# Performance work log

Measured on AMD Instinct MI355X. Metric: run time of the kernel, lower is better.

The kernel has to match this reference:

```python
import jax, jax.numpy as jnp
import numpy as np

EPS_NORM = 1e-12   # torch F.normalize eps
GN_EPS = 1e-5      # GroupNorm eps
FACTOR = 5
NUM_HEADS = 8
NEG_SLOPE = 0.01   # LeakyReLU default


def _l2norm(x, axis):
    n = jnp.sqrt(jnp.sum(x * x, axis=axis, keepdims=True))
    return x / jnp.maximum(n, EPS_NORM)


def setup_inputs() -> dict:
    key = jax.random.key(0)
    B, C, H, W, D = 2, 256, 16, 16, 16
    N = H * W * D
    sample_k = FACTOR * int(np.ceil(np.log(N)))  # 45
    ks = jax.random.split(key, 8)
    s = 0.02
    return {
        "x": jax.random.normal(ks[0], (B, C, H, W, D), jnp.float32),
        "W_qkvv": jax.random.normal(ks[1], (C, 4 * C), jnp.float32) * s,
        "W_out": jax.random.normal(ks[2], (C, C), jnp.float32) * s,
        "b_out": jnp.zeros((C,), jnp.float32),
        "W_out2": jax.random.normal(ks[3], (C, C), jnp.float32) * s,
        "b_out2": jnp.zeros((C,), jnp.float32),
        "gamma1": 0.1 * jnp.ones((C,), jnp.float32),
        "conv_w": jax.random.normal(ks[4], (C, C, 3, 3, 3), jnp.float32) * s,
        "gn_w": jnp.ones((C,), jnp.float32),
        "gn_b": jnp.zeros((C,), jnp.float32),
        "index_sample": jax.random.randint(ks[5], (N, sample_k), 0, N),
    }


def reference(x, W_qkvv, W_out, b_out, W_out2, b_out2, gamma1, conv_w, gn_w, gn_b, index_sample):
    B, C, H, Wd, D = x.shape
    N = H * Wd * D
    nh = NUM_HEADS
    dh = C // nh
    xs = x.reshape(B, C, N).transpose(0, 2, 1)                    # [B,N,C]
    qkvv = (xs @ W_qkvv).reshape(B, N, 4, nh, dh).transpose(2, 0, 3, 1, 4)  # [4,B,nh,N,dh]
    q, k, v_ca, v_sa = qkvv[0], qkvv[1], qkvv[2], qkvv[3]
    q = _l2norm(q, axis=-2)   # normalize over sequence dim (dim=-2 in torch)
    k = _l2norm(k, axis=-2)

    u = FACTOR * int(np.ceil(np.log(N)))
    # --- ProbSparse _prob_QK ---
    K_sample = k[:, :, index_sample, :]                            # [B,nh,N,sk,dh]
    QK_sample = jnp.einsum('bhle,bhlse->bhls', q, K_sample)        # [B,nh,N,sk]
    M = QK_sample.max(-1) - QK_sample.sum(-1) / N                  # sparsity measure
    _, M_top = jax.lax.top_k(M, u)                                 # [B,nh,u]
    b_idx = jnp.arange(B)[:, None, None]
    h_idx = jnp.arange(nh)[None, :, None]
    Q_red = q[b_idx, h_idx, M_top]                                 # [B,nh,u,dh]
    scores = jnp.einsum('bhud,bhld->bhul', Q_red, k)               # [B,nh,u,N]

    # --- spatial (ProbSparse) context ---
    ctx = jnp.broadcast_to(v_sa.mean(axis=-2, keepdims=True), v_sa.shape)  # [B,nh,N,dh]
    attn_sa = jax.nn.softmax(scores, axis=-1)
    upd = jnp.einsum('bhul,bhld->bhud', attn_sa, v_sa)             # [B,nh,u,dh]
    ctx = ctx.at[b_idx, h_idx, M_top].set(upd)

    # --- channel attention (on transposed q,k,v: [B,nh,dh,N]) ---
    qt = q.transpose(0, 1, 3, 2)
    kt = k.transpose(0, 1, 3, 2)
    vt = v_ca.transpose(0, 1, 3, 2)
    attn_ca = jax.nn.softmax(jnp.einsum('bhdn,bhen->bhde', qt, kt), axis=-1)  # [B,nh,dh,dh]
    x_ca = jnp.einsum('bhde,bhen->bhdn', attn_ca, vt).transpose(0, 3, 1, 2).reshape(B, N, C)
    x_sa = ctx.transpose(0, 3, 1, 2).reshape(B, N, C)              # matches source permute
    x_sa = x_sa @ W_out + b_out                                    # dead branch (source discards)
    x_ca = x_ca @ W_out2 + b_out2
    epa = x_ca  # source: x = x_SA + x_CA; x = x_CA  -> only CA branch survives

    attn = xs + gamma1 * epa                                       # [B,N,C]
    attn = attn.reshape(B, H, Wd, D, C).transpose(0, 4, 1, 2, 3)   # [B,C,H,W,D]

    # conv8: Dropout3d (eval=id) -> Conv3d(3x3x3, no bias) -> GroupNorm(1 group)
    y = jax.lax.conv_general_dilated(attn, conv_w, (1, 1, 1), [(1, 1)] * 3,
                                     dimension_numbers=('NCDHW', 'OIDHW', 'NCDHW'))
    mu = y.mean(axis=(1, 2, 3, 4), keepdims=True)
    var = y.var(axis=(1, 2, 3, 4), keepdims=True)
    y = (y - mu) / jnp.sqrt(var + GN_EPS)
    y = y * gn_w[None, :, None, None, None] + gn_b[None, :, None, None, None]
    y = y + attn
    return jnp.where(y >= 0, y, NEG_SLOPE * y)
```

## Files before the change

### kernel.cpp

```cpp
#include <hip/hip_runtime.h>
#include <hip/hip_bf16.h>
#include <stdint.h>


#define B_ 2
#define C_ 256
#define N_ 4096
#define NH 8
#define PADV 5832
#define CN  (C_*N_)
#define BCN (B_*CN)

typedef unsigned short u16;
typedef unsigned int   u32;

using frag16 = __attribute__((ext_vector_type(8))) short;
using f32x4  = __attribute__((ext_vector_type(4))) float;

__device__ __forceinline__ u16 f2bf(float f) {
    u32 u = __float_as_uint(f);
    u += 0x7fff + ((u >> 16) & 1);
    return (u16)(u >> 16);
}
__device__ __forceinline__ float bb(u16 h) { return __uint_as_float((u32)h << 16); }
__device__ __forceinline__ void gld16(const void* g, void* l) {
    __builtin_amdgcn_global_load_lds((const __attribute__((address_space(1))) u32*)g,
                                     (__attribute__((address_space(3))) u32*)l, 16, 0, 0);
}
__device__ __forceinline__ int padrow(int n) {
    int z = n >> 8, y = (n >> 4) & 15, x = n & 15;
    return (z + 1) * 324 + (y + 1) * 18 + (x + 1);
}

#define OFF_TB    0
#define OFF_SP    3145728
#define OFF_XCAB  3670016
#define OFF_PKB   0
#define OFF_Y     3145728
#define OFF_ATTB  6291456
#define OFF_ATTP  7340032
#define OFF_WT2   8833024
#define OFF_W2B   9717760
#define OFF_WQB   9750528
#define OFF_XT    9848832
#define OFF_RSQ   10897408
#define OFF_RED   10898432

__global__ __launch_bounds__(256) void k_prep(const float* __restrict__ CW, const float* __restrict__ W2,
                                              const float* __restrict__ Wq, const float* __restrict__ X,
                                              u16* __restrict__ WT2, u16* __restrict__ W2B,
                                              u16* __restrict__ Wqb, u16* __restrict__ XT,
                                              u32* __restrict__ APz, float* __restrict__ RSQ) {
    __shared__ __align__(16) float ls[6912];
    float (*ts)[33] = (float(*)[33])ls;
    int blk = blockIdx.x, tid = threadIdx.x;
    if (blk < 256) {
        int co = blk;
        const float* src = CW + (size_t)co * 6912;
        for (int u = tid; u < 6912; u += 256) ls[u] = src[u];
        __syncthreads();
#pragma unroll
        for (int t = 0; t < 27; ++t)
            WT2[(((size_t)t * 256 + co) << 8) + tid] = f2bf(ls[tid * 27 + t]);
    } else if (blk < 320) {
        int bi = blk - 256; int c0 = (bi & 7) * 32, p0 = (bi >> 3) * 32;
        int tx = tid & 31, ty = tid >> 5;
#pragma unroll
        for (int i = 0; i < 4; ++i) ts[ty + i * 8][tx] = W2[(size_t)(p0 + ty + i * 8) * 256 + c0 + tx];
        __syncthreads();
#pragma unroll
        for (int i = 0; i < 4; ++i) W2B[(size_t)(c0 + ty + i * 8) * 256 + p0 + tx] = f2bf(ts[tx][ty + i * 8]);
    } else if (blk < 512) {
        int bi = blk - 320; int c0 = (bi & 7) * 32, j0 = (bi >> 3) * 32;
        int tx = tid & 31, ty = tid >> 5;
#pragma unroll
        for (int i = 0; i < 4; ++i) ts[ty + i * 8][tx] = Wq[(size_t)(c0 + ty + i * 8) * 1024 + j0 + tx];
        __syncthreads();
#pragma unroll
        for (int i = 0; i < 4; ++i) Wqb[(size_t)(j0 + ty + i * 8) * 256 + c0 + tx] = f2bf(ts[tx][ty + i * 8]);
    } else if (blk < 2560) {
        int idx = blk - 512;
        int n0 = (idx & 127) * 32, c0 = ((idx >> 7) & 7) * 32, b = idx >> 10;
        int tx = tid & 31, ty = tid >> 5;
        const float* Xb = X + (size_t)b * CN;
#pragma unroll
        for (int i = 0; i < 4; ++i) ts[ty + i * 8][tx] = Xb[(size_t)(c0 + ty + i * 8) * N_ + n0 + tx];
        __syncthreads();
        u16* Xo = XT + (size_t)b * N_ * C_;
#pragma unroll
        for (int i = 0; i < 4; ++i) Xo[(size_t)(n0 + ty + i * 8) * C_ + c0 + tx] = f2bf(ts[tx][ty + i * 8]);
    } else if (blk < 8392) {
        APz[(size_t)(blk - 2560) * 256 + tid] = 0;
    } else {
        ((float4*)RSQ)[tid] = make_float4(0.f, 0.f, 0.f, 0.f);
    }
}

__global__ __launch_bounds__(256) void k_qkv_mfma(const u16* __restrict__ Wqb, const u16* __restrict__ XT,
                                                  u16* __restrict__ Tb, float* __restrict__ RSQ) {
    __shared__ __align__(16) u16 As[2][8192], Bs[2][8192];
    int n0 = blockIdx.x * 128, j0 = blockIdx.y * 128, b = blockIdx.z;
    int tid = threadIdx.x, lane = tid & 63, w = tid >> 6;
    int wm = w & 1, wn = w >> 1, qm = lane >> 4, lm = lane & 15;
    int srow = lane >> 3;
    int sperm = (((lane & 7) ^ srow) << 3);
    const u16* aB = Wqb + ((size_t)(j0 + w * 32 + srow) << 8) + sperm;
    const u16* bB = XT + ((size_t)(b * N_ + n0 + w * 32 + srow) << 8) + sperm;
    int rdp = ((lm & 7) << 3);
    f32x4 acc[4][4] = {};
    auto stg = [&](int p, int kc) {
#pragma unroll
        for (int i = 0; i < 4; ++i) {
            gld16(aB + i * 2048 + kc * 64, &As[p][w * 2048 + i * 512]);
            gld16(bB + i * 2048 + kc * 64, &Bs[p][w * 2048 + i * 512]);
        }
    };
    stg(0, 0);
#pragma unroll
    for (int kt = 0; kt < 4; ++kt) {
        int p = kt & 1;
        __syncthreads();
        if (kt < 3) stg(p ^ 1, kt + 1);
#pragma unroll
        for (int c2 = 0; c2 < 2; ++c2) {
            frag16 af[4], bf[4];
#pragma unroll
            for (int i = 0; i < 4; ++i)
                af[i] = *(const frag16*)&As[p][(wm * 64 + i * 16 + lm) * 64 + ((((c2 * 4 + qm) << 3) ^ rdp))];
#pragma unroll
            for (int j = 0; j < 4; ++j)
                bf[j] = *(const frag16*)&Bs[p][(wn * 64 + j * 16 + lm) * 64 + ((((c2 * 4 + qm) << 3) ^ rdp))];
#pragma unroll
            for (int i = 0; i < 4; ++i)
#pragma unroll
                for (int j = 0; j < 4; ++j)
                    acc[i][j] = __builtin_amdgcn_mfma_f32_16x16x32_bf16(af[i], bf[j], acc[i][j], 0, 0, 0);
        }
    }
    u16* To = Tb + ((size_t)b * 768 + j0 + wm * 64) * N_ + n0 + wn * 64;
#pragma unroll
    for (int i = 0; i < 4; ++i)
#pragma unroll
        for (int j = 0; j < 4; ++j)
#pragma unroll
            for (int r = 0; r < 4; ++r)
                To[(size_t)(i * 16 + qm * 4 + r) * N_ + j * 16 + lm] = f2bf(acc[i][j][r]);
    if (j0 < 512) {
#pragma unroll
        for (int i = 0; i < 4; ++i)
#pragma unroll
            for (int r = 0; r < 4; ++r) {
                float s = 0.f;
#pragma unroll
                for (int j = 0; j < 4; ++j) s += acc[i][j][r] * acc[i][j][r];
                s += __shfl_xor(s, 1); s += __shfl_xor(s, 2);
                s += __shfl_xor(s, 4); s += __shfl_xor(s, 8);
                if (lm == 0)
                    atomicAdd(&RSQ[b * 512 + j0 + wm * 64 + i * 16 + qm * 4 + r], s);
            }
    }
}

__global__ __launch_bounds__(256) void k_ca_part(const u16* __restrict__ Tb, float* __restrict__ SP) {
    int s = blockIdx.x, h = blockIdx.y, b = blockIdx.z;
    int t = threadIdx.x, d = t & 31, eg = t >> 5;
    const u16* Q  = Tb + ((size_t)b * 768 + h * 32 + d) * N_ + s * 128;
    const u16* K0 = Tb + ((size_t)b * 768 + 256 + h * 32 + eg * 4) * N_ + s * 128;
    float a0 = 0.f, a1 = 0.f, a2 = 0.f, a3 = 0.f;
    for (int u = 0; u < 128; u += 8) {
        uint4 qv = *(const uint4*)(Q + u);
        uint4 k0 = *(const uint4*)(K0 + u);
        uint4 k1 = *(const uint4*)(K0 + (size_t)N_ + u);
        uint4 k2 = *(const uint4*)(K0 + (size_t)2 * N_ + u);
        uint4 k3 = *(const uint4*)(K0 + (size_t)3 * N_ + u);
        const u16 *qh = (const u16*)&qv, *h0 = (const u16*)&k0, *h1 = (const u16*)&k1,
                  *h2 = (const u16*)&k2, *h3 = (const u16*)&k3;
#pragma unroll
        for (int i = 0; i < 8; ++i) {
            float qf = bb(qh[i]);
            a0 += qf * bb(h0[i]); a1 += qf * bb(h1[i]);
            a2 += qf * bb(h2[i]); a3 += qf * bb(h3[i]);
        }
    }
    float* o = SP + (((size_t)(b * NH + h)) * 32 + s) * 1024 + d * 32 + eg * 4;
    o[0] = a0; o[1] = a1; o[2] = a2; o[3] = a3;
}

__global__ __launch_bounds__(256) void k_ca_apply(const u16* __restrict__ Tb, const float* __restrict__ SP,
                                                  const float* __restrict__ RSQ, u16* __restrict__ XCAb) {
    int n0 = blockIdx.x * 256, h = blockIdx.y, b = blockIdx.z;
    __shared__ float raw[1024];
    __shared__ float Ae[32][32];
    __shared__ float sq[32], sk[32];
    int tid = threadIdx.x;
    const float* Sp = SP + ((size_t)(b * NH + h)) * 32768;
    for (int u = tid; u < 1024; u += 256) {
        float v = 0.f;
#pragma unroll
        for (int s = 0; s < 32; ++s) v += Sp[s * 1024 + u];
        raw[u] = v;
    }
    if (tid < 32) {
        sq[tid] = 1.0f / fmaxf(sqrtf(RSQ[b * 512 + h * 32 + tid]), 1e-12f);
        sk[tid] = 1.0f / fmaxf(sqrtf(RSQ[b * 512 + 256 + h * 32 + tid]), 1e-12f);
    }
    __syncthreads();
    if (tid < 32) {
        float iq = sq[tid];
        float sv[32]; float m = -1e30f;
#pragma unroll
        for (int e = 0; e < 32; ++e) { sv[e] = raw[tid * 32 + e] * iq * sk[e]; m = fmaxf(m, sv[e]); }
        float sm = 0.f;
#pragma unroll
        for (int e = 0; e < 32; ++e) { sv[e] = __expf(sv[e] - m); sm += sv[e]; }
        float rinv = 1.0f / sm;
#pragma unroll
        for (int e = 0; e < 32; ++e) Ae[e][tid] = sv[e] * rinv;
    }
    __syncthreads();
    int n = n0 + tid;
    const u16* V = Tb + ((size_t)b * 768 + 512 + h * 32) * N_ + n;
    float acc[32];
#pragma unroll
    for (int d = 0; d < 32; ++d) acc[d] = 0.f;
#pragma unroll
    for (int e = 0; e < 32; ++e) {
        float v = bb(V[(size_t)e * N_]);
#pragma unroll
        for (int dg = 0; dg < 8; ++dg) {
            float4 a4 = *(const float4*)&Ae[e][dg * 4];
            acc[dg * 4 + 0] += a4.x * v; acc[dg * 4 + 1] += a4.y * v;
            acc[dg * 4 + 2] += a4.z * v; acc[dg * 4 + 3] += a4.w * v;
        }
    }
    u16* o = XCAb + ((size_t)b * N_ + n) * C_ + h * 32;
#pragma unroll
    for (int dg = 0; dg < 8; ++dg) {
        ushort4 pk;
        pk.x = f2bf(acc[dg * 4 + 0]); pk.y = f2bf(acc[dg * 4 + 1]);
        pk.z = f2bf(acc[dg * 4 + 2]); pk.w = f2bf(acc[dg * 4 + 3]);
        *(ushort4*)(o + dg * 4) = pk;
    }
}

__global__ __launch_bounds__(256) void k_out2_mfma(const u16* __restrict__ W2B, const u16* __restrict__ XCAb,
                                                   const float* __restrict__ bias2, const float* __restrict__ g1,
                                                   const float* __restrict__ X, u16* __restrict__ ATTb,
                                                   u16* __restrict__ ATTp) {
    __shared__ __align__(16) u16 As[2][8192], Bs[2][8192];
    int n0 = blockIdx.x * 128, c0 = blockIdx.y * 128, b = blockIdx.z;
    int tid = threadIdx.x, lane = tid & 63, w = tid >> 6;
    int wm = w & 1, wn = w >> 1, qm = lane >> 4, lm = lane & 15;
    int srow = lane >> 3;
    int sperm = (((lane & 7) ^ srow) << 3);
    const u16* aB = W2B + ((size_t)(c0 + w * 32 + srow) << 8) + sperm;
    const u16* bB = XCAb + ((size_t)(b * N_ + n0 + w * 32 + srow) << 8) + sperm;
    int rdp = ((lm & 7) << 3);
    f32x4 acc[4][4] = {};
    auto stg = [&](int p, int kc) {
#pragma unroll
        for (int i = 0; i < 4; ++i) {
            gld16(aB + i * 2048 + kc * 64, &As[p][w * 2048 + i * 512]);
            gld16(bB + i * 2048 + kc * 64, &Bs[p][w * 2048 + i * 512]);
        }
    };
    stg(0, 0);
#pragma unroll
    for (int kt = 0; kt < 4; ++kt) {
        int p = kt & 1;
        __syncthreads();
        if (kt < 3) stg(p ^ 1, kt + 1);
#pragma unroll
        for (int c2 = 0; c2 < 2; ++c2) {
            frag16 af[4], bf[4];
#pragma unroll
            for (int i = 0; i < 4; ++i)
                af[i] = *(const frag16*)&As[p][(wm * 64 + i * 16 + lm) * 64 + ((((c2 * 4 + qm) << 3) ^ rdp))];
#pragma unroll
            for (int j = 0; j < 4; ++j)
                bf[j] = *(const frag16*)&Bs[p][(wn * 64 + j * 16 + lm) * 64 + ((((c2 * 4 + qm) << 3) ^ rdp))];
#pragma unroll
            for (int i = 0; i < 4; ++i)
#pragma unroll
                for (int j = 0; j < 4; ++j)
                    acc[i][j] = __builtin_amdgcn_mfma_f32_16x16x32_bf16(af[i], bf[j], acc[i][j], 0, 0, 0);
        }
    }
    int c_base = c0 + wm * 64, n_base = n0 + wn * 64;
    const float* xin = X + (size_t)b * CN;
    u16* Ao = ATTb + (size_t)b * CN;
    u16* Ap = ATTp + ((size_t)b * PADV << 8);
    float val[4][4][4];
#pragma unroll
    for (int i = 0; i < 4; ++i)
#pragma unroll
        for (int r = 0; r < 4; ++r) {
            int c = c_base + i * 16 + qm * 4 + r;
            float gv = g1[c], bi = bias2[c];
#pragma unroll
            for (int j = 0; j < 4; ++j) {
                int n = n_base + j * 16 + lm;
                float v = xin[(size_t)c * N_ + n] + gv * (acc[i][j][r] + bi);
                val[i][j][r] = v;
                Ao[(size_t)c * N_ + n] = f2bf(v);
            }
        }
#pragma unroll
    for (int j = 0; j < 4; ++j) {
        int n = n_base + j * 16 + lm;
        int pr = padrow(n);
#pragma unroll
        for (int i = 0; i < 4; ++i) {
            ushort4 pk;
            pk.x = f2bf(val[i][j][0]); pk.y = f2bf(val[i][j][1]);
            pk.z = f2bf(val[i][j][2]); pk.w = f2bf(val[i][j][3]);
            *(ushort4*)&Ap[((size_t)pr << 8) + c_base + i * 16 + qm * 4] = pk;
        }
    }
}

__global__ __launch_bounds__(256) void k_conv_mfma(const u16* __restrict__ WT2, const u16* __restrict__ ATTp,
                                                   u16* __restrict__ Pk) {
    __shared__ __align__(16) u16 As[2][8192], Bs[2][8192];
    int n0 = blockIdx.x * 128;
    int co0 = (blockIdx.y & 1) * 128, ks = blockIdx.y >> 1;
    int b = blockIdx.z;
    int tid = threadIdx.x, lane = tid & 63, w = tid >> 6;
    int wm = w & 1, wn = w >> 1, qm = lane >> 4, lm = lane & 15;
    int srow = lane >> 3;
    int sperm = (((lane & 7) ^ srow) << 3);
    const u16* aB = WT2 + (((size_t)ks * 9 * 256 + co0 + w * 32 + srow) << 8) + sperm;
    int prA[4];
#pragma unroll
    for (int i = 0; i < 4; ++i) prA[i] = padrow(n0 + w * 32 + i * 8 + srow) << 8;
    const u16* bB = ATTp + ((size_t)b * PADV << 8) + ((ks - 1) * 324 << 8) + sperm;
    int rdp = ((lm & 7) << 3);
    f32x4 acc[4][4] = {};
    auto stg = [&](int p, int kt) {
        int tap9 = kt >> 2, kc = kt & 3;
        int K9 = ((tap9 / 3) - 1) * 18 + (tap9 % 3 - 1);
#pragma unroll
        for (int i = 0; i < 4; ++i) {
            gld16(aB + (size_t)tap9 * 65536 + i * 2048 + kc * 64, &As[p][w * 2048 + i * 512]);
            gld16(bB + prA[i] + K9 * 256 + kc * 64,              &Bs[p][w * 2048 + i * 512]);
        }
    };
    stg(0, 0);
#pragma unroll
    for (int kt = 0; kt < 36; ++kt) {
        int p = kt & 1;
        __syncthreads();
        if (kt < 35) stg(p ^ 1, kt + 1);
#pragma unroll
        for (int c2 = 0; c2 < 2; ++c2) {
            frag16 af[4], bf[4];
#pragma unroll
            for (int i = 0; i < 4; ++i)
                af[i] = *(const frag16*)&As[p][(wm * 64 + i * 16 + lm) * 64 + ((((c2 * 4 + qm) << 3) ^ rdp))];
#pragma unroll
            for (int j = 0; j < 4; ++j)
                bf[j] = *(const frag16*)&Bs[p][(wn * 64 + j * 16 + lm) * 64 + ((((c2 * 4 + qm) << 3) ^ rdp))];
#pragma unroll
            for (int i = 0; i < 4; ++i)
#pragma unroll
                for (int j = 0; j < 4; ++j)
                    acc[i][j] = __builtin_amdgcn_mfma_f32_16x16x32_bf16(af[i], bf[j], acc[i][j], 0, 0, 0);
        }
    }
    u16* Pb = Pk + ((size_t)(ks * B_ + b) * C_ + co0 + wm * 64) * N_ + n0 + wn * 64;
#pragma unroll
    for (int i = 0; i < 4; ++i)
#pragma unroll
        for (int j = 0; j < 4; ++j)
#pragma unroll
            for (int r = 0; r < 4; ++r)
                Pb[(size_t)(i * 16 + qm * 4 + r) * N_ + j * 16 + lm] = f2bf(acc[i][j][r]);
}

__global__ __launch_bounds__(256) void k_gn_reduce(const u16* __restrict__ Pk, u16* __restrict__ Y,
                                                   float* __restrict__ RED) {
    int blk = blockIdx.x, b = blockIdx.y;
    size_t base = (size_t)b * CN + (size_t)blk * 16384;
    const u16* p0 = Pk + base;
    const u16* p1 = Pk + BCN + base;
    const u16* p2 = Pk + (size_t)2 * BCN + base;
    u16* y = Y + base;
    float s = 0.f, q = 0.f;
    for (int u = threadIdx.x * 8; u < 16384; u += 2048) {
        uint4 a = *(const uint4*)&p0[u];
        uint4 c1 = *(const uint4*)&p1[u];
        uint4 c2 = *(const uint4*)&p2[u];
        const u16 *A = (const u16*)&a, *B1 = (const u16*)&c1, *C2 = (const u16*)&c2;
        __align__(16) u16 outp[8];
#pragma unroll
        for (int i = 0; i < 8; ++i) {
            float v = bb(A[i]) + bb(B1[i]) + bb(C2[i]);
            s += v; q += v * v;
            outp[i] = f2bf(v);
        }
        *(uint4*)&y[u] = *(const uint4*)outp;
    }
#pragma unroll
    for (int off = 32; off; off >>= 1) { s += __shfl_down(s, off); q += __shfl_down(q, off); }
    __shared__ float rs_[4], rq[4];
    int lane = threadIdx.x & 63, wv = threadIdx.x >> 6;
    if (!lane) { rs_[wv] = s; rq[wv] = q; }
    __syncthreads();
    if (threadIdx.x == 0) {
        RED[((size_t)b * 64 + blk) * 2 + 0] = rs_[0] + rs_[1] + rs_[2] + rs_[3];
        RED[((size_t)b * 64 + blk) * 2 + 1] = rq[0] + rq[1] + rq[2] + rq[3];
    }
}

__global__ __launch_bounds__(256) void k_final(const u16* __restrict__ Y, const u16* __restrict__ ATTb,
                                               const float* __restrict__ RED, const float* __restrict__ gw,
                                               const float* __restrict__ gb, float* __restrict__ out) {
    int i = blockIdx.x * 256 + threadIdx.x;
    int b = i >> 20;
    int c = (i >> 12) & 255;
    __shared__ float smu[2];
    if (threadIdx.x < 64) {
        float s = RED[((size_t)b * 64 + threadIdx.x) * 2 + 0];
        float q = RED[((size_t)b * 64 + threadIdx.x) * 2 + 1];
#pragma unroll
        for (int off = 32; off; off >>= 1) { s += __shfl_down(s, off); q += __shfl_down(q, off); }
        if (threadIdx.x == 0) {
            float inv = 1.0f / (float)CN;
            float mu = s * inv, var = q * inv - mu * mu;
            smu[0] = mu; smu[1] = rsqrtf(var + 1e-5f);
        }
    }
    __syncthreads();
    float v = (bb(Y[i]) - smu[0]) * smu[1] * gw[c] + gb[c] + bb(ATTb[i]);
    out[i] = v >= 0.f ? v : 0.01f * v;
}

extern "C" void kernel_launch(void* const* d_in, const int* in_sizes, int n_in,
                              void* d_out, int out_size, void* d_ws, size_t ws_size,
                              hipStream_t stream) {
    const float* x      = (const float*)d_in[0];
    const float* Wqkvv  = (const float*)d_in[1];
    const float* W_out2 = (const float*)d_in[4];
    const float* b_out2 = (const float*)d_in[5];
    const float* gamma1 = (const float*)d_in[6];
    const float* conv_w = (const float*)d_in[7];
    const float* gn_w   = (const float*)d_in[8];
    const float* gn_b   = (const float*)d_in[9];
    float* out = (float*)d_out;
    float* ws = (float*)d_ws;

    u16*   Tb   = (u16*)(ws + OFF_TB);
    float* SP   = ws + OFF_SP;
    u16*   XCAb = (u16*)(ws + OFF_XCAB);
    u16*   Pk   = (u16*)(ws + OFF_PKB);
    u16*   Y    = (u16*)(ws + OFF_Y);
    u16*   ATTb = (u16*)(ws + OFF_ATTB);
    u16*   ATTp = (u16*)(ws + OFF_ATTP);
    u16*   WT2  = (u16*)(ws + OFF_WT2);
    u16*   W2B  = (u16*)(ws + OFF_W2B);
    u16*   Wqb  = (u16*)(ws + OFF_WQB);
    u16*   XT   = (u16*)(ws + OFF_XT);
    float* RSQ  = ws + OFF_RSQ;
    float* RED  = ws + OFF_RED;

    k_prep      <<<8393, 256, 0, stream>>>(conv_w, W_out2, Wqkvv, x, WT2, W2B, Wqb, XT, (u32*)ATTp, RSQ);
    k_qkv_mfma  <<<dim3(N_ / 128, 6, B_), 256, 0, stream>>>(Wqb, XT, Tb, RSQ);
    k_ca_part   <<<dim3(32, NH, B_), 256, 0, stream>>>(Tb, SP);
    k_ca_apply  <<<dim3(N_ / 256, NH, B_), 256, 0, stream>>>(Tb, SP, RSQ, XCAb);
    k_out2_mfma <<<dim3(N_ / 128, C_ / 128, B_), 256, 0, stream>>>(W2B, XCAb, b_out2, gamma1, x, ATTb, ATTp);
    k_conv_mfma <<<dim3(N_ / 128, 6, B_), 256, 0, stream>>>(WT2, ATTp, Pk);
    k_gn_reduce <<<dim3(64, B_), 256, 0, stream>>>(Pk, Y, RED);
    k_final     <<<(B_ * CN) / 256, 256, 0, stream>>>(Y, ATTb, RED, gn_w, gn_b, out);
}
```

Measured before the change: 181.2 us.

## Compute channel-attention scores with MFMA and enlarge X transpose tiles

```diff
diff --git a/kernel.cpp b/kernel.cpp
--- a/kernel.cpp
+++ b/kernel.cpp
@@ -53,6 +53,7 @@
                                               u32* __restrict__ APz, float* __restrict__ RSQ) {
     __shared__ __align__(16) float ls[6912];
     float (*ts)[33] = (float(*)[33])ls;
+    float (*t64)[65] = (float(*)[65])ls;
     int blk = blockIdx.x, tid = threadIdx.x;
     if (blk < 256) {
         int co = blk;
@@ -78,19 +79,20 @@
         __syncthreads();
 #pragma unroll
         for (int i = 0; i < 4; ++i) Wqb[(size_t)(j0 + ty + i * 8) * 256 + c0 + tx] = f2bf(ts[tx][ty + i * 8]);
-    } else if (blk < 2560) {
+    } else if (blk < 1024) {
         int idx = blk - 512;
-        int n0 = (idx & 127) * 32, c0 = ((idx >> 7) & 7) * 32, b = idx >> 10;
-        int tx = tid & 31, ty = tid >> 5;
+        int n0 = (idx & 63) * 64, c0 = ((idx >> 6) & 3) * 64, b = idx >> 8;
+        int tn = tid & 63, tc4 = tid >> 6;
         const float* Xb = X + (size_t)b * CN;
 #pragma unroll
-        for (int i = 0; i < 4; ++i) ts[ty + i * 8][tx] = Xb[(size_t)(c0 + ty + i * 8) * N_ + n0 + tx];
+        for (int i = 0; i < 16; ++i) t64[tc4 + i * 4][tn] = Xb[(size_t)(c0 + tc4 + i * 4) * N_ + n0 + tn];
         __syncthreads();
         u16* Xo = XT + (size_t)b * N_ * C_;
 #pragma unroll
-        for (int i = 0; i < 4; ++i) Xo[(size_t)(n0 + ty + i * 8) * C_ + c0 + tx] = f2bf(ts[tx][ty + i * 8]);
-    } else if (blk < 8392) {
-        APz[(size_t)(blk - 2560) * 256 + tid] = 0;
+        for (int i = 0; i < 16; ++i)
+            Xo[(size_t)(n0 + tc4 + i * 4) * C_ + c0 + tn] = f2bf(t64[tn][tc4 + i * 4]);
+    } else if (blk < 6856) {
+        APz[(size_t)(blk - 1024) * 256 + tid] = 0;
     } else {
         ((float4*)RSQ)[tid] = make_float4(0.f, 0.f, 0.f, 0.f);
     }
@@ -161,29 +163,45 @@
     }
 }
 
-__global__ __launch_bounds__(256) void k_ca_part(const u16* __restrict__ Tb, float* __restrict__ SP) {
-    int s = blockIdx.x, h = blockIdx.y, b = blockIdx.z;
-    int t = threadIdx.x, d = t & 31, eg = t >> 5;
-    const u16* Q  = Tb + ((size_t)b * 768 + h * 32 + d) * N_ + s * 128;
-    const u16* K0 = Tb + ((size_t)b * 768 + 256 + h * 32 + eg * 4) * N_ + s * 128;
-    float a0 = 0.f, a1 = 0.f, a2 = 0.f, a3 = 0.f;
-    for (int u = 0; u < 128; u += 8) {
-        uint4 qv = *(const uint4*)(Q + u);
-        uint4 k0 = *(const uint4*)(K0 + u);
-        uint4 k1 = *(const uint4*)(K0 + (size_t)N_ + u);
-        uint4 k2 = *(const uint4*)(K0 + (size_t)2 * N_ + u);
-        uint4 k3 = *(const uint4*)(K0 + (size_t)3 * N_ + u);
-        const u16 *qh = (const u16*)&qv, *h0 = (const u16*)&k0, *h1 = (const u16*)&k1,
-                  *h2 = (const u16*)&k2, *h3 = (const u16*)&k3;
-#pragma unroll
-        for (int i = 0; i < 8; ++i) {
-            float qf = bb(qh[i]);
-            a0 += qf * bb(h0[i]); a1 += qf * bb(h1[i]);
-            a2 += qf * bb(h2[i]); a3 += qf * bb(h3[i]);
-        }
-    }
-    float* o = SP + (((size_t)(b * NH + h)) * 32 + s) * 1024 + d * 32 + eg * 4;
-    o[0] = a0; o[1] = a1; o[2] = a2; o[3] = a3;
+__global__ __launch_bounds__(256) void k_ca_score(const u16* __restrict__ Tb, float* __restrict__ SP) {
+    __shared__ __align__(16) u16 Qs[2][8192], Ks[2][8192];
+    int ks = blockIdx.x, h = blockIdx.y, b = blockIdx.z;
+    int tid = threadIdx.x, lane = tid & 63, w = tid >> 6;
+    int wm = w & 1, wn = w >> 1, qm = lane >> 4, lm = lane & 15;
+    const u16* Qb = Tb + ((size_t)b * 768 + h * 32) * N_;
+    const u16* Kb = Tb + ((size_t)b * 768 + 256 + h * 32) * N_;
+    int k0base = ks * 512;
+    auto stg = [&](int p, int ck) {
+        int k0 = k0base + ck * 256;
+#pragma unroll
+        for (int ri = 0; ri < 4; ++ri) {
+            int row = ri * 8 + w * 2 + (lane >> 5);
+            int cg = (lane & 31) ^ (row & 31);
+            gld16(Qb + (size_t)row * N_ + k0 + cg * 8, &Qs[p][ri * 2048 + w * 512]);
+            gld16(Kb + (size_t)row * N_ + k0 + cg * 8, &Ks[p][ri * 2048 + w * 512]);
+        }
+    };
+    f32x4 acc = {};
+    stg(0, 0);
+#pragma unroll
+    for (int ck = 0; ck < 2; ++ck) {
+        int p = ck & 1;
+        __syncthreads();
+        if (ck < 1) stg(p ^ 1, ck + 1);
+        int rowA = wm * 16 + lm, rowB = wn * 16 + lm;
+#pragma unroll
+        for (int kk = 0; kk < 8; ++kk) {
+            int slotA = ((kk * 4 + qm) ^ (rowA & 31)) << 3;
+            int slotB = ((kk * 4 + qm) ^ (rowB & 31)) << 3;
+            frag16 af = *(const frag16*)&Qs[p][rowA * 256 + slotA];
+            frag16 bf = *(const frag16*)&Ks[p][rowB * 256 + slotB];
+            acc = __builtin_amdgcn_mfma_f32_16x16x32_bf16(af, bf, acc, 0, 0, 0);
+        }
+    }
+    float* o = SP + (((size_t)(b * NH + h)) * 8 + ks) * 1024;
+#pragma unroll
+    for (int r = 0; r < 4; ++r)
+        o[(wm * 16 + qm * 4 + r) * 32 + wn * 16 + lm] = acc[r];
 }
 
 __global__ __launch_bounds__(256) void k_ca_apply(const u16* __restrict__ Tb, const float* __restrict__ SP,
@@ -193,11 +211,11 @@
     __shared__ float Ae[32][32];
     __shared__ float sq[32], sk[32];
     int tid = threadIdx.x;
-    const float* Sp = SP + ((size_t)(b * NH + h)) * 32768;
+    const float* Sp = SP + ((size_t)(b * NH + h)) * 8192;
     for (int u = tid; u < 1024; u += 256) {
         float v = 0.f;
 #pragma unroll
-        for (int s = 0; s < 32; ++s) v += Sp[s * 1024 + u];
+        for (int s = 0; s < 8; ++s) v += Sp[s * 1024 + u];
         raw[u] = v;
     }
     if (tid < 32) {
@@ -463,9 +481,9 @@
     float* RSQ  = ws + OFF_RSQ;
     float* RED  = ws + OFF_RED;
 
-    k_prep      <<<8393, 256, 0, stream>>>(conv_w, W_out2, Wqkvv, x, WT2, W2B, Wqb, XT, (u32*)ATTp, RSQ);
+    k_prep      <<<6857, 256, 0, stream>>>(conv_w, W_out2, Wqkvv, x, WT2, W2B, Wqb, XT, (u32*)ATTp, RSQ);
     k_qkv_mfma  <<<dim3(N_ / 128, 6, B_), 256, 0, stream>>>(Wqb, XT, Tb, RSQ);
-    k_ca_part   <<<dim3(32, NH, B_), 256, 0, stream>>>(Tb, SP);
+    k_ca_score  <<<dim3(8, NH, B_), 256, 0, stream>>>(Tb, SP);
     k_ca_apply  <<<dim3(N_ / 256, NH, B_), 256, 0, stream>>>(Tb, SP, RSQ, XCAb);
     k_out2_mfma <<<dim3(N_ / 128, C_ / 128, B_), 256, 0, stream>>>(W2B, XCAb, b_out2, gamma1, x, ATTb, ATTp);
     k_conv_mfma <<<dim3(N_ / 128, 6, B_), 256, 0, stream>>>(WT2, ATTp, Pk);
```

New measurement: 174.1 us. -3.9%, faster.
